# Kernel optimization log

Measured on AMD Instinct MI355X. Metric: run time of the kernel, lower is better.

Reference implementation:

```python
import jax, jax.numpy as jnp
import numpy as np
import math

B, S_IN, S_OUT, D_IN, D_OUT, G = 8, 1024, 1024, 96, 96, 8
LN_EPS = 1e-5


def setup_inputs() -> dict:
    key = jax.random.key(0)
    k_x, k_m, k_p, k_l = jax.random.split(key, 4)
    x = jax.random.normal(k_x, (B, S_IN, D_IN), dtype=jnp.float32)
    M = jax.random.uniform(k_m, (D_OUT, D_IN), minval=-0.5, maxval=0.5, dtype=jnp.float32)
    P = jax.random.uniform(k_p, (D_OUT, D_OUT, G), minval=-0.1, maxval=0.1, dtype=jnp.float32)
    Linker = jax.random.uniform(k_l, (S_IN, S_OUT), minval=-0.1, maxval=0.1, dtype=jnp.float32)
    gamma = jnp.ones((D_OUT,), dtype=jnp.float32)
    beta = jnp.zeros((D_OUT,), dtype=jnp.float32)
    return {"x": x, "M": M, "P": P, "Linker": Linker, "gamma": gamma, "beta": beta}


def _layer_norm(z, gamma, beta):
    mu = jnp.mean(z, axis=-1, keepdims=True)
    var = jnp.mean(jnp.square(z - mu), axis=-1, keepdims=True)
    return (z - mu) * jax.lax.rsqrt(var + LN_EPS) * gamma + beta


def reference(x, M, P, Linker, gamma, beta):
    # Z = x @ M^T, then LayerNorm over feature dim
    Z0 = jnp.einsum('bsj,ij->bsi', x, M)           # (B, S_in, D_out)
    Z = _layer_norm(Z0, gamma, beta)
    # periods[i,j,g] = i*(D_out*G) + j*G + g + 2
    periods = (jnp.arange(D_OUT * D_OUT * G, dtype=jnp.float32)
               .reshape(D_OUT, D_OUT, G) + 2.0)
    k = jnp.arange(S_IN, dtype=jnp.float32)
    # phi[s,i,j,g] = cos(2*pi*s / periods[i,j,g])
    phi = jnp.cos((2.0 * math.pi) * k[:, None, None, None] / periods[None])
    # fuse basis reduction: W[s,i,j] = sum_g P[i,j,g] * phi[s,i,j,g]
    W = jnp.einsum('sijg,ijg->sij', phi, P)        # (S_in, D_out, D_out)
    # T[b,s,i] = sum_j Z[b,s,j] * W[s,i,j]
    T = jnp.einsum('bsj,sij->bsi', Z, W)           # (B, S_in, D_out)
    # sequence transform via Linker
    U = jnp.einsum('bsi,st->bti', T, Linker)       # (B, S_out, D_out)
    # shared residual: x @ M^T (pre-LN) through the same Linker
    residual = jnp.einsum('bsi,st->bti', Z0, Linker)
    return U + residual
```

## Files before the change

### kernel.cpp

```cpp
#include <hip/hip_runtime.h>
#include <cstdint>
#include <cstddef>

#define BSTRIDE 98304

typedef __attribute__((ext_vector_type(8))) short short8;
typedef __attribute__((ext_vector_type(4))) float f32x4;

__device__ __forceinline__ uint16_t f2bf(float x) {
    uint32_t u = __float_as_uint(x);
    return (uint16_t)((u + 0x7FFF + ((u >> 16) & 1)) >> 16);
}
__device__ __forceinline__ float bf2f(uint16_t b) {
    return __uint_as_float(((uint32_t)b) << 16);
}

union SmemA {
    struct {
        union {
            float M[96][97];
            struct { float zb[16][97]; float ps1[16][8];
                     float ps2[16][8]; float stats[16][2]; } ln;
        } m;
        float xs[16][96];
    } a;
    struct { float T[64][65]; } kl;
};

__global__ __launch_bounds__(384, 4) void kA(
    const float* __restrict__ x, const float* __restrict__ M,
    const float* __restrict__ L,
    const float* __restrict__ gamma, const float* __restrict__ beta,
    float* __restrict__ Z0, float* __restrict__ Z, uint16_t* __restrict__ Lt)
{
    __shared__ SmemA sm;
    const int t  = threadIdx.x;
    const int bx = blockIdx.x;

    if (bx >= 512) {
        const int bx2 = bx - 512;
        const int s0 = (bx2 & 15) * 64, t0 = (bx2 >> 4) * 64;
        if (t < 64) {
            for (int r = 0; r < 64; ++r)
                sm.kl.T[r][t] = L[(size_t)(s0 + r) * 1024 + t0 + t];
        }
        __syncthreads();
        if (t < 64) {
            uint16_t* orow = Lt + (size_t)(t0 + t) * 1024 + s0;
            #pragma unroll
            for (int c4 = 0; c4 < 16; ++c4) {
                uint32_t u01 = (uint32_t)f2bf(sm.kl.T[c4*4+0][t]) |
                               ((uint32_t)f2bf(sm.kl.T[c4*4+1][t]) << 16);
                uint32_t u23 = (uint32_t)f2bf(sm.kl.T[c4*4+2][t]) |
                               ((uint32_t)f2bf(sm.kl.T[c4*4+3][t]) << 16);
                uint2 o; o.x = u01; o.y = u23;
                *(uint2*)(orow + c4 * 4) = o;
            }
        }
        return;
    }

    const int R0 = bx * 16;
    const int b  = R0 >> 10;
    const int sb = R0 & 1023;

    #pragma unroll
    for (int k = 0; k < 6; ++k) {
        int mm = t + 384 * k;
        int i = mm / 24, j0 = (mm % 24) * 4;
        float4 v = *(const float4*)(M + (size_t)i * 96 + j0);
        sm.a.m.M[i][j0]   = v.x; sm.a.m.M[i][j0+1] = v.y;
        sm.a.m.M[i][j0+2] = v.z; sm.a.m.M[i][j0+3] = v.w;
    }
    {
        int row = t / 24, j0 = (t % 24) * 4;
        float4 v = *(const float4*)(x + (size_t)(R0 + row) * 96 + j0);
        *(float4*)&sm.a.xs[row][j0] = v;
    }
    __syncthreads();

    const int e = t % 96;
    const int q = t / 96;
    float acc[4] = {0.f, 0.f, 0.f, 0.f};
    for (int j0 = 0; j0 < 96; j0 += 4) {
        float m0 = sm.a.m.M[e][j0+0], m1 = sm.a.m.M[e][j0+1];
        float m2 = sm.a.m.M[e][j0+2], m3 = sm.a.m.M[e][j0+3];
        #pragma unroll
        for (int rr = 0; rr < 4; ++rr) {
            float4 xv = *(const float4*)&sm.a.xs[q * 4 + rr][j0];
            acc[rr] = fmaf(m0, xv.x, fmaf(m1, xv.y,
                      fmaf(m2, xv.z, fmaf(m3, xv.w, acc[rr]))));
        }
    }
    __syncthreads();
    #pragma unroll
    for (int rr = 0; rr < 4; ++rr) sm.a.m.ln.zb[q * 4 + rr][e] = acc[rr];
    __syncthreads();

    if (t < 128) {
        int r = t >> 3, seg = t & 7;
        float s1 = 0.f, s2 = 0.f;
        #pragma unroll
        for (int k = 0; k < 12; ++k) {
            float v = sm.a.m.ln.zb[r][seg * 12 + k];
            s1 += v; s2 += v * v;
        }
        sm.a.m.ln.ps1[r][seg] = s1; sm.a.m.ln.ps2[r][seg] = s2;
    }
    __syncthreads();
    if (t < 16) {
        float s1 = 0.f, s2 = 0.f;
        #pragma unroll
        for (int k = 0; k < 8; ++k) { s1 += sm.a.m.ln.ps1[t][k]; s2 += sm.a.m.ln.ps2[t][k]; }
        float mu  = s1 * (1.f / 96.f);
        float var = s2 * (1.f / 96.f) - mu * mu;
        sm.a.m.ln.stats[t][0] = mu;
        sm.a.m.ln.stats[t][1] = rsqrtf(var + 1e-5f);
    }
    __syncthreads();

    {
        float gm = gamma[e], bt = beta[e];
        #pragma unroll
        for (int rr = 0; rr < 4; ++rr) {
            int r = q * 4 + rr;
            float z  = acc[rr];
            float mu = sm.a.m.ln.stats[r][0], rs = sm.a.m.ln.stats[r][1];
            size_t o = (size_t)(sb + r) * 768 + (size_t)b * 96 + e;
            Z0[o] = z;
            Z[o]  = (z - mu) * rs * gm + bt;
        }
    }
}

struct SmemB {
    float    zs[8][8][100];
    uint16_t W[8][12][104];
    uint16_t stage[12][8][8];
};

__global__ __launch_bounds__(384, 4) void kB(
    const float* __restrict__ P, const float* __restrict__ Z,
    const float* __restrict__ Z0, uint16_t* __restrict__ Vt)
{
    __shared__ SmemB sm;
    const int t  = threadIdx.x;
    const int sg = blockIdx.x & 127;
    const int ih = blockIdx.x >> 7;
    const int s0 = sg * 8;
    const int i0 = ih * 12;

    #pragma unroll
    for (int k = 0; k < 4; ++k) {
        int c = t + 384 * k;
        int elem = c * 4;
        int sp = elem / 768, rem = elem - sp * 768;
        int bb = rem / 96,  j0 = rem - bb * 96;
        float4 v = *(const float4*)(Z + (size_t)s0 * 768 + elem);
        *(float4*)&sm.zs[sp][bb][j0] = v;
    }

    {
        const int j   = t % 96;
        const int iqb = t / 96;
        const float sf  = (float)s0;
        const float sm1 = sf - 1.0f;
        #pragma unroll 1
        for (int kk = 0; kk < 3; ++kk) {
            const int ip = kk * 4 + iqb;
            const int ig = i0 + ip;
            const float* Pp = P + ((size_t)ig * 96 + j) * 8;
            float4 pa = *(const float4*)(Pp);
            float4 pb = *(const float4*)(Pp + 4);
            float pv[8] = {pa.x, pa.y, pa.z, pa.w, pb.x, pb.y, pb.z, pb.w};
            float base = (float)((ig * 96 + j) * 8 + 2);
            float c[8], cp[8], tc[8];
            #pragma unroll
            for (int g = 0; g < 8; ++g) {
                float inv = __builtin_amdgcn_rcpf(base + (float)g);
                tc[g] = 2.0f * __builtin_amdgcn_cosf(inv);
                c[g]  = __builtin_amdgcn_cosf(__builtin_amdgcn_fractf(sf  * inv));
                cp[g] = __builtin_amdgcn_cosf(__builtin_amdgcn_fractf(sm1 * inv));
            }
            #pragma unroll
            for (int sp = 0; sp < 8; ++sp) {
                float w = 0.f;
                #pragma unroll
                for (int g = 0; g < 8; ++g) w = fmaf(pv[g], c[g], w);
                sm.W[sp][ip][j] = f2bf(w);
                #pragma unroll
                for (int g = 0; g < 8; ++g) {
                    float cn = fmaf(tc[g], c[g], -cp[g]);
                    cp[g] = c[g]; c[g] = cn;
                }
            }
        }
    }
    __syncthreads();

    {
        const int s2  = t / 48;
        const int rem = t % 48;
        const int ipq = rem / 8;
        const int bb  = rem % 8;
        const int ia  = ipq * 2, ib = ia + 1;
        float accA = 0.f, accB = 0.f;
        const uint16_t* w0 = &sm.W[s2][ia][0];
        const uint16_t* w1 = &sm.W[s2][ib][0];
        const float*    zz = &sm.zs[s2][bb][0];
        #pragma unroll 3
        for (int j0 = 0; j0 < 96; j0 += 8) {
            short8 wa = *(const short8*)(w0 + j0);
            short8 wb = *(const short8*)(w1 + j0);
            float4 z0 = *(const float4*)(zz + j0);
            float4 z1 = *(const float4*)(zz + j0 + 4);
            accA = fmaf(bf2f((uint16_t)wa[0]), z0.x, accA);
            accB = fmaf(bf2f((uint16_t)wb[0]), z0.x, accB);
            accA = fmaf(bf2f((uint16_t)wa[1]), z0.y, accA);
            accB = fmaf(bf2f((uint16_t)wb[1]), z0.y, accB);
            accA = fmaf(bf2f((uint16_t)wa[2]), z0.z, accA);
            accB = fmaf(bf2f((uint16_t)wb[2]), z0.z, accB);
            accA = fmaf(bf2f((uint16_t)wa[3]), z0.w, accA);
            accB = fmaf(bf2f((uint16_t)wb[3]), z0.w, accB);
            accA = fmaf(bf2f((uint16_t)wa[4]), z1.x, accA);
            accB = fmaf(bf2f((uint16_t)wb[4]), z1.x, accB);
            accA = fmaf(bf2f((uint16_t)wa[5]), z1.y, accA);
            accB = fmaf(bf2f((uint16_t)wb[5]), z1.y, accB);
            accA = fmaf(bf2f((uint16_t)wa[6]), z1.z, accA);
            accB = fmaf(bf2f((uint16_t)wb[6]), z1.z, accB);
            accA = fmaf(bf2f((uint16_t)wa[7]), z1.w, accA);
            accB = fmaf(bf2f((uint16_t)wb[7]), z1.w, accB);
        }
        float2 r2 = *(const float2*)(Z0 + (size_t)(s0 + s2) * 768 + bb * 96 + i0 + ia);
        sm.stage[ia][bb][s2] = f2bf(accA + r2.x);
        sm.stage[ib][bb][s2] = f2bf(accB + r2.y);
    }
    __syncthreads();

    if (t < 96) {
        int ip = t >> 3, bb = t & 7;
        uint4 v = *(const uint4*)&sm.stage[ip][bb][0];
        *(uint4*)(Vt + ((size_t)sg * 768 + (size_t)bb * 96 + i0 + ip) * 8) = v;
    }
}

__global__ __launch_bounds__(256, 4) void k3_mfma(
    const uint16_t* __restrict__ Lt, const uint16_t* __restrict__ Vt,
    float* __restrict__ out)
{
    __shared__ float racc[3][64][13];
    const int lane = threadIdx.x & 63;
    const int kw   = threadIdx.x >> 6;
    const int m    = lane & 15;
    const int quad = lane >> 4;
    const int t0   = blockIdx.x * 16;
    const int b    = blockIdx.y;
    const int ih   = blockIdx.z;

    const uint16_t* Lp = Lt + (size_t)(t0 + m) * 1024 + kw * 256 + quad * 8;
    const uint16_t* Vp = Vt + ((size_t)(kw * 32 + quad) * 768 +
                               (size_t)b * 96 + ih * 48 + m) * 8;

    f32x4 acc[3];
    #pragma unroll
    for (int ii = 0; ii < 3; ++ii) acc[ii] = (f32x4){0.f, 0.f, 0.f, 0.f};

    short8 a = *(const short8*)Lp;
    short8 bv[3];
    #pragma unroll
    for (int ii = 0; ii < 3; ++ii)
        bv[ii] = *(const short8*)(Vp + ii * 128);

    for (int kc = 0; kc < 7; ++kc) {
        short8 an = *(const short8*)(Lp + (kc + 1) * 32);
        short8 bn[3];
        #pragma unroll
        for (int ii = 0; ii < 3; ++ii)
            bn[ii] = *(const short8*)(Vp + (size_t)(kc + 1) * 24576 + ii * 128);
        #pragma unroll
        for (int ii = 0; ii < 3; ++ii)
            acc[ii] = __builtin_amdgcn_mfma_f32_16x16x32_bf16(a, bv[ii], acc[ii], 0, 0, 0);
        a = an;
        #pragma unroll
        for (int ii = 0; ii < 3; ++ii) bv[ii] = bn[ii];
    }
    #pragma unroll
    for (int ii = 0; ii < 3; ++ii)
        acc[ii] = __builtin_amdgcn_mfma_f32_16x16x32_bf16(a, bv[ii], acc[ii], 0, 0, 0);

    if (kw > 0) {
        #pragma unroll
        for (int ii = 0; ii < 3; ++ii)
            #pragma unroll
            for (int r = 0; r < 4; ++r)
                racc[kw - 1][lane][ii * 4 + r] = acc[ii][r];
    }
    __syncthreads();
    if (kw == 0) {
        float* po = out + (size_t)b * BSTRIDE;
        #pragma unroll
        for (int ii = 0; ii < 3; ++ii)
            #pragma unroll
            for (int r = 0; r < 4; ++r)
                po[(size_t)(t0 + quad * 4 + r) * 96 + ih * 48 + ii * 16 + m] =
                    acc[ii][r] + racc[0][lane][ii * 4 + r] +
                    racc[1][lane][ii * 4 + r] + racc[2][lane][ii * 4 + r];
    }
}

extern "C" void kernel_launch(void* const* d_in, const int* in_sizes, int n_in,
                              void* d_out, int out_size, void* d_ws, size_t ws_size,
                              hipStream_t stream)
{
    const float* x     = (const float*)d_in[0];
    const float* M     = (const float*)d_in[1];
    const float* P     = (const float*)d_in[2];
    const float* Lnk   = (const float*)d_in[3];
    const float* gamma = (const float*)d_in[4];
    const float* beta  = (const float*)d_in[5];
    float* out = (float*)d_out;

    uint8_t* ws = (uint8_t*)d_ws;
    uint16_t* Lt = (uint16_t*)ws;
    uint16_t* Vt = (uint16_t*)(ws + 2097152);
    float*    Z0 = (float*)(ws + 3670016);
    float*    Z  = (float*)(ws + 6815744);

    kA<<<768, 384, 0, stream>>>(x, M, Lnk, gamma, beta, Z0, Z, Lt);
    kB<<<1024, 384, 0, stream>>>(P, Z, Z0, Vt);
    k3_mfma<<<dim3(64, 8, 2), 256, 0, stream>>>(Lt, Vt, out);
}
```

Before: 105.9 us.

## Fuse three kernels into one cooperative persistent kernel with grid syncs

Merges the projection/LayerNorm/Linker-transpose stage, the W-basis/T stage and the MFMA Linker GEMM into a single cooperative kernel of 768 blocks, separated by grid.sync barriers. Later stages loop over their original work units with a stride of the grid size. The aim is to remove the launch gaps and tail effects between three separate kernels. In exchange it adds the cost of grid-wide barriers, and it requires 768 blocks of 384 threads to be co-resident (at least 3 per CU) or it falls back to the old three-launch path. Stages 2 and 3 now run 1024 work units over 768 blocks, so some blocks process two units, which is less balanced than before.

```diff
diff --git a/kernel.cpp b/kernel.cpp
--- a/kernel.cpp
+++ b/kernel.cpp
@@ -1,6 +1,9 @@
 #include <hip/hip_runtime.h>
+#include <hip/hip_cooperative_groups.h>
 #include <cstdint>
 #include <cstddef>
+
+namespace cg = cooperative_groups;
 
 #define BSTRIDE 98304
 
@@ -15,15 +18,305 @@
     return __uint_as_float(((uint32_t)b) << 16);
 }
 
+struct SmemA_ {
+    union {
+        float M[96][97];
+        struct { float zb[16][97]; float ps1[16][8];
+                 float ps2[16][8]; float stats[16][2]; } ln;
+    } m;
+    float xs[16][96];
+};
+struct SmemB_ {
+    float    zs[8][8][100];
+    uint16_t W[8][12][104];
+    uint16_t stage[12][8][8];
+};
+union SmemU {
+    SmemA_ a;
+    SmemB_ b;
+    float  racc[3][64][13];
+    float  T[64][65];
+};
+
+__global__ __launch_bounds__(384, 5) void mega(
+    const float* __restrict__ x, const float* __restrict__ M,
+    const float* __restrict__ P, const float* __restrict__ L,
+    const float* __restrict__ gamma, const float* __restrict__ beta,
+    float* __restrict__ Z0, float* __restrict__ Z,
+    uint16_t* __restrict__ Lt, uint16_t* __restrict__ Vt,
+    float* __restrict__ out)
+{
+    __shared__ SmemU sm;
+    const int t  = threadIdx.x;
+    const int bx = blockIdx.x;
+    cg::grid_group grid = cg::this_grid();
+
+    if (bx >= 512) {
+        const int bx2 = bx - 512;
+        const int s0 = (bx2 & 15) * 64, t0 = (bx2 >> 4) * 64;
+        if (t < 64) {
+            for (int r = 0; r < 64; ++r)
+                sm.T[r][t] = L[(size_t)(s0 + r) * 1024 + t0 + t];
+        }
+        __syncthreads();
+        if (t < 64) {
+            uint16_t* orow = Lt + (size_t)(t0 + t) * 1024 + s0;
+            #pragma unroll
+            for (int c4 = 0; c4 < 16; ++c4) {
+                uint32_t u01 = (uint32_t)f2bf(sm.T[c4*4+0][t]) |
+                               ((uint32_t)f2bf(sm.T[c4*4+1][t]) << 16);
+                uint32_t u23 = (uint32_t)f2bf(sm.T[c4*4+2][t]) |
+                               ((uint32_t)f2bf(sm.T[c4*4+3][t]) << 16);
+                uint2 o; o.x = u01; o.y = u23;
+                *(uint2*)(orow + c4 * 4) = o;
+            }
+        }
+    } else {
+        const int R0 = bx * 16;
+        const int b  = R0 >> 10;
+        const int sb = R0 & 1023;
+
+        #pragma unroll
+        for (int k = 0; k < 6; ++k) {
+            int mm = t + 384 * k;
+            int i = mm / 24, j0 = (mm % 24) * 4;
+            float4 v = *(const float4*)(M + (size_t)i * 96 + j0);
+            sm.a.m.M[i][j0]   = v.x; sm.a.m.M[i][j0+1] = v.y;
+            sm.a.m.M[i][j0+2] = v.z; sm.a.m.M[i][j0+3] = v.w;
+        }
+        {
+            int row = t / 24, j0 = (t % 24) * 4;
+            float4 v = *(const float4*)(x + (size_t)(R0 + row) * 96 + j0);
+            *(float4*)&sm.a.xs[row][j0] = v;
+        }
+        __syncthreads();
+
+        const int e = t % 96;
+        const int q = t / 96;
+        float acc[4] = {0.f, 0.f, 0.f, 0.f};
+        for (int j0 = 0; j0 < 96; j0 += 4) {
+            float m0 = sm.a.m.M[e][j0+0], m1 = sm.a.m.M[e][j0+1];
+            float m2 = sm.a.m.M[e][j0+2], m3 = sm.a.m.M[e][j0+3];
+            #pragma unroll
+            for (int rr = 0; rr < 4; ++rr) {
+                float4 xv = *(const float4*)&sm.a.xs[q * 4 + rr][j0];
+                acc[rr] = fmaf(m0, xv.x, fmaf(m1, xv.y,
+                          fmaf(m2, xv.z, fmaf(m3, xv.w, acc[rr]))));
+            }
+        }
+        __syncthreads();
+        #pragma unroll
+        for (int rr = 0; rr < 4; ++rr) sm.a.m.ln.zb[q * 4 + rr][e] = acc[rr];
+        __syncthreads();
+
+        if (t < 128) {
+            int r = t >> 3, seg = t & 7;
+            float s1 = 0.f, s2 = 0.f;
+            #pragma unroll
+            for (int k = 0; k < 12; ++k) {
+                float v = sm.a.m.ln.zb[r][seg * 12 + k];
+                s1 += v; s2 += v * v;
+            }
+            sm.a.m.ln.ps1[r][seg] = s1; sm.a.m.ln.ps2[r][seg] = s2;
+        }
+        __syncthreads();
+        if (t < 16) {
+            float s1 = 0.f, s2 = 0.f;
+            #pragma unroll
+            for (int k = 0; k < 8; ++k) { s1 += sm.a.m.ln.ps1[t][k]; s2 += sm.a.m.ln.ps2[t][k]; }
+            float mu  = s1 * (1.f / 96.f);
+            float var = s2 * (1.f / 96.f) - mu * mu;
+            sm.a.m.ln.stats[t][0] = mu;
+            sm.a.m.ln.stats[t][1] = rsqrtf(var + 1e-5f);
+        }
+        __syncthreads();
+        {
+            float gm = gamma[e], bt = beta[e];
+            #pragma unroll
+            for (int rr = 0; rr < 4; ++rr) {
+                int r = q * 4 + rr;
+                float z  = acc[rr];
+                float mu = sm.a.m.ln.stats[r][0], rs = sm.a.m.ln.stats[r][1];
+                size_t o = (size_t)(sb + r) * 768 + (size_t)b * 96 + e;
+                Z0[o] = z;
+                Z[o]  = (z - mu) * rs * gm + bt;
+            }
+        }
+    }
+
+    __threadfence();
+    grid.sync();
+
+    for (int u = bx; u < 1024; u += 768) {
+        const int sg = u & 127;
+        const int ih = u >> 7;
+        const int s0 = sg * 8;
+        const int i0 = ih * 12;
+
+        #pragma unroll
+        for (int k = 0; k < 4; ++k) {
+            int c = t + 384 * k;
+            int elem = c * 4;
+            int sp = elem / 768, rem = elem - sp * 768;
+            int bb = rem / 96,  j0 = rem - bb * 96;
+            float4 v = *(const float4*)(Z + (size_t)s0 * 768 + elem);
+            *(float4*)&sm.b.zs[sp][bb][j0] = v;
+        }
+
+        {
+            const int j   = t % 96;
+            const int iqb = t / 96;
+            const float sf  = (float)s0;
+            const float sm1 = sf - 1.0f;
+            #pragma unroll 1
+            for (int kk = 0; kk < 3; ++kk) {
+                const int ip = kk * 4 + iqb;
+                const int ig = i0 + ip;
+                const float* Pp = P + ((size_t)ig * 96 + j) * 8;
+                float4 pa = *(const float4*)(Pp);
+                float4 pb = *(const float4*)(Pp + 4);
+                float pv[8] = {pa.x, pa.y, pa.z, pa.w, pb.x, pb.y, pb.z, pb.w};
+                float base = (float)((ig * 96 + j) * 8 + 2);
+                float c[8], cp[8], tc[8];
+                #pragma unroll
+                for (int g = 0; g < 8; ++g) {
+                    float inv = __builtin_amdgcn_rcpf(base + (float)g);
+                    tc[g] = 2.0f * __builtin_amdgcn_cosf(inv);
+                    c[g]  = __builtin_amdgcn_cosf(__builtin_amdgcn_fractf(sf  * inv));
+                    cp[g] = __builtin_amdgcn_cosf(__builtin_amdgcn_fractf(sm1 * inv));
+                }
+                #pragma unroll
+                for (int sp = 0; sp < 8; ++sp) {
+                    float w = 0.f;
+                    #pragma unroll
+                    for (int g = 0; g < 8; ++g) w = fmaf(pv[g], c[g], w);
+                    sm.b.W[sp][ip][j] = f2bf(w);
+                    #pragma unroll
+                    for (int g = 0; g < 8; ++g) {
+                        float cn = fmaf(tc[g], c[g], -cp[g]);
+                        cp[g] = c[g]; c[g] = cn;
+                    }
+                }
+            }
+        }
+        __syncthreads();
+
+        {
+            const int s2  = t / 48;
+            const int rem = t % 48;
+            const int ipq = rem / 8;
+            const int bb  = rem % 8;
+            const int ia  = ipq * 2, ib = ia + 1;
+            float accA = 0.f, accB = 0.f;
+            const uint16_t* w0 = &sm.b.W[s2][ia][0];
+            const uint16_t* w1 = &sm.b.W[s2][ib][0];
+            const float*    zz = &sm.b.zs[s2][bb][0];
+            #pragma unroll 3
+            for (int j0 = 0; j0 < 96; j0 += 8) {
+                short8 wa = *(const short8*)(w0 + j0);
+                short8 wb = *(const short8*)(w1 + j0);
+                float4 z0 = *(const float4*)(zz + j0);
+                float4 z1 = *(const float4*)(zz + j0 + 4);
+                accA = fmaf(bf2f((uint16_t)wa[0]), z0.x, accA);
+                accB = fmaf(bf2f((uint16_t)wb[0]), z0.x, accB);
+                accA = fmaf(bf2f((uint16_t)wa[1]), z0.y, accA);
+                accB = fmaf(bf2f((uint16_t)wb[1]), z0.y, accB);
+                accA = fmaf(bf2f((uint16_t)wa[2]), z0.z, accA);
+                accB = fmaf(bf2f((uint16_t)wb[2]), z0.z, accB);
+                accA = fmaf(bf2f((uint16_t)wa[3]), z0.w, accA);
+                accB = fmaf(bf2f((uint16_t)wb[3]), z0.w, accB);
+                accA = fmaf(bf2f((uint16_t)wa[4]), z1.x, accA);
+                accB = fmaf(bf2f((uint16_t)wb[4]), z1.x, accB);
+                accA = fmaf(bf2f((uint16_t)wa[5]), z1.y, accA);
+                accB = fmaf(bf2f((uint16_t)wb[5]), z1.y, accB);
+                accA = fmaf(bf2f((uint16_t)wa[6]), z1.z, accA);
+                accB = fmaf(bf2f((uint16_t)wb[6]), z1.z, accB);
+                accA = fmaf(bf2f((uint16_t)wa[7]), z1.w, accA);
+                accB = fmaf(bf2f((uint16_t)wb[7]), z1.w, accB);
+            }
+            float2 r2 = *(const float2*)(Z0 + (size_t)(s0 + s2) * 768 + bb * 96 + i0 + ia);
+            sm.b.stage[ia][bb][s2] = f2bf(accA + r2.x);
+            sm.b.stage[ib][bb][s2] = f2bf(accB + r2.y);
+        }
+        __syncthreads();
+
+        if (t < 96) {
+            int ip = t >> 3, bb = t & 7;
+            uint4 v = *(const uint4*)&sm.b.stage[ip][bb][0];
+            *(uint4*)(Vt + ((size_t)sg * 768 + (size_t)bb * 96 + i0 + ip) * 8) = v;
+        }
+    }
+
+    __threadfence();
+    grid.sync();
+
+    for (int u = bx; u < 1024; u += 768) {
+        const int tq  = u & 63;
+        const int b   = (u >> 6) & 7;
+        const int ih2 = u >> 9;
+        const bool act = (t < 256);
+        const int lane = t & 63;
+        const int kw   = (t >> 6) & 3;
+        const int m    = lane & 15;
+        const int quad = lane >> 4;
+        const int t0   = tq * 16;
+
+        f32x4 acc3[3];
+        #pragma unroll
+        for (int ii = 0; ii < 3; ++ii) acc3[ii] = (f32x4){0.f, 0.f, 0.f, 0.f};
+
+        if (act) {
+            const uint16_t* Lp = Lt + (size_t)(t0 + m) * 1024 + kw * 256 + quad * 8;
+            const uint16_t* Vp = Vt + ((size_t)(kw * 32 + quad) * 768 +
+                                       (size_t)b * 96 + ih2 * 48 + m) * 8;
+            short8 a = *(const short8*)Lp;
+            short8 bv[3];
+            #pragma unroll
+            for (int ii = 0; ii < 3; ++ii)
+                bv[ii] = *(const short8*)(Vp + ii * 128);
+
+            for (int kc = 0; kc < 7; ++kc) {
+                short8 an = *(const short8*)(Lp + (kc + 1) * 32);
+                short8 bn[3];
+                #pragma unroll
+                for (int ii = 0; ii < 3; ++ii)
+                    bn[ii] = *(const short8*)(Vp + (size_t)(kc + 1) * 24576 + ii * 128);
+                #pragma unroll
+                for (int ii = 0; ii < 3; ++ii)
+                    acc3[ii] = __builtin_amdgcn_mfma_f32_16x16x32_bf16(a, bv[ii], acc3[ii], 0, 0, 0);
+                a = an;
+                #pragma unroll
+                for (int ii = 0; ii < 3; ++ii) bv[ii] = bn[ii];
+            }
+            #pragma unroll
+            for (int ii = 0; ii < 3; ++ii)
+                acc3[ii] = __builtin_amdgcn_mfma_f32_16x16x32_bf16(a, bv[ii], acc3[ii], 0, 0, 0);
+
+            if (kw > 0) {
+                #pragma unroll
+                for (int ii = 0; ii < 3; ++ii)
+                    #pragma unroll
+                    for (int r = 0; r < 4; ++r)
+                        sm.racc[kw - 1][lane][ii * 4 + r] = acc3[ii][r];
+            }
+        }
+        __syncthreads();
+        if (act && kw == 0) {
+            float* po = out + (size_t)b * BSTRIDE;
+            #pragma unroll
+            for (int ii = 0; ii < 3; ++ii)
+                #pragma unroll
+                for (int r = 0; r < 4; ++r)
+                    po[(size_t)(t0 + quad * 4 + r) * 96 + ih2 * 48 + ii * 16 + m] =
+                        acc3[ii][r] + sm.racc[0][lane][ii * 4 + r] +
+                        sm.racc[1][lane][ii * 4 + r] + sm.racc[2][lane][ii * 4 + r];
+        }
+        __syncthreads();
+    }
+}
+
 union SmemA {
-    struct {
-        union {
-            float M[96][97];
-            struct { float zb[16][97]; float ps1[16][8];
-                     float ps2[16][8]; float stats[16][2]; } ln;
-        } m;
-        float xs[16][96];
-    } a;
+    SmemA_ a;
     struct { float T[64][65]; } kl;
 };
 
@@ -133,17 +426,11 @@
     }
 }
 
-struct SmemB {
-    float    zs[8][8][100];
-    uint16_t W[8][12][104];
-    uint16_t stage[12][8][8];
-};
-
 __global__ __launch_bounds__(384, 4) void kB(
     const float* __restrict__ P, const float* __restrict__ Z,
     const float* __restrict__ Z0, uint16_t* __restrict__ Vt)
 {
-    __shared__ SmemB sm;
+    __shared__ SmemB_ sm;
     const int t  = threadIdx.x;
     const int sg = blockIdx.x & 127;
     const int ih = blockIdx.x >> 7;
@@ -326,7 +613,30 @@
     float*    Z0 = (float*)(ws + 3670016);
     float*    Z  = (float*)(ws + 6815744);
 
-    kA<<<768, 384, 0, stream>>>(x, M, Lnk, gamma, beta, Z0, Z, Lt);
-    kB<<<1024, 384, 0, stream>>>(P, Z, Z0, Vt);
-    k3_mfma<<<dim3(64, 8, 2), 256, 0, stream>>>(Lt, Vt, out);
+    static int coop_state = -1;
+    if (coop_state == -1) {
+        int nb = 0;
+        hipError_t e = hipOccupancyMaxActiveBlocksPerMultiprocessor(
+            &nb, reinterpret_cast<const void*>(mega), 384, 0);
+        coop_state = (e == hipSuccess && nb >= 3) ? 1 : 0;
+    }
+
+    bool launched = false;
+    if (coop_state == 1) {
+        void* args[] = {
+            (void*)&x, (void*)&M, (void*)&P, (void*)&Lnk,
+            (void*)&gamma, (void*)&beta,
+            (void*)&Z0, (void*)&Z, (void*)&Lt, (void*)&Vt, (void*)&out
+        };
+        hipError_t e = hipLaunchCooperativeKernel(
+            reinterpret_cast<const void*>(mega), dim3(768), dim3(384),
+            args, 0, stream);
+        if (e == hipSuccess) launched = true;
+        else coop_state = 0;
+    }
+    if (!launched) {
+        kA<<<768, 384, 0, stream>>>(x, M, Lnk, gamma, beta, Z0, Z, Lt);
+        kB<<<1024, 384, 0, stream>>>(P, Z, Z0, Vt);
+        k3_mfma<<<dim3(64, 8, 2), 256, 0, stream>>>(Lt, Vt, out);
+    }
 }
```

After: 105.8 us. About the same (-0.1%).
